# Performance work log

Measured on AMD Instinct MI355X. Metric: run time of the kernel, lower is better.

Reference implementation:

```python
import jax, jax.numpy as jnp
import numpy as np

WK = 5        # fine_window_size
STRIDE = 4    # hardcoded in forward
PAD = WK // 2


def _gather_windows(feat, b, idx):
    # feat: [N, C, H, W]; b, idx: [M]. Replicates F.unfold(k=5, s=4, p=2)
    # followed by permute/reshape(n, l, W^2, c) and advanced indexing,
    # but only materializes the M selected windows (fused unfold+gather).
    N, C, H, W = feat.shape
    out_w = (W + 2 * PAD - WK) // STRIDE + 1
    fp = jnp.pad(feat, ((0, 0), (0, 0), (PAD, PAD), (PAD, PAD)))
    gy = idx // out_w
    gx = idx % out_w
    rows = gy[:, None] * STRIDE + jnp.arange(WK)   # [M, WK]
    cols = gx[:, None] * STRIDE + jnp.arange(WK)   # [M, WK]
    # advanced indices at axes 0,2,3 with slice at axis 1 -> [M, WK, WK, C]
    patch = fp[b[:, None, None], :, rows[:, :, None], cols[:, None, :]]
    # F.unfold flattens channel-major (C, kh, kw); the torch code then
    # reshapes that C*WK*WK axis as (WK*WK, C) -- an index-mixing reshape
    # we must replicate exactly.
    M = b.shape[0]
    patch = patch.transpose(0, 3, 1, 2).reshape(M, C * WK * WK)
    return patch.reshape(M, WK * WK, C)


def setup_inputs() -> dict:
    key = jax.random.key(0)
    k0, k1, kb, ki, kj = jax.random.split(key, 5)
    N, C, H, W = 4, 128, 240, 320
    L = (H // STRIDE) * (W // STRIDE)  # 4800 coarse positions
    M = 6000
    return {
        "feat_f0": jax.random.normal(k0, (N, C, H, W), dtype=jnp.float32),
        "feat_f1": jax.random.normal(k1, (N, C, H, W), dtype=jnp.float32),
        "hw0_f": jnp.array([H, W], dtype=jnp.int64),
        "hw0_c": jnp.array([H // STRIDE, W // STRIDE], dtype=jnp.int64),
        "b_ids": jax.random.randint(kb, (M,), 0, N, dtype=jnp.int64),
        "i_ids": jax.random.randint(ki, (M,), 0, L, dtype=jnp.int64),
        "j_ids": jax.random.randint(kj, (M,), 0, L, dtype=jnp.int64),
    }


def reference(feat_f0, feat_f1, hw0_f, hw0_c, b_ids, i_ids, j_ids):
    feat0 = _gather_windows(feat_f0, b_ids, i_ids)  # [M, W^2, C]
    feat1 = _gather_windows(feat_f1, b_ids, j_ids)  # [M, W^2, C]
    return feat0, feat1
```

## Files before the change

### kernel.cpp

```cpp
#include <hip/hip_runtime.h>


#define MPTS 6000
#define NCH  128
#define FH   240
#define FW   320
#define OUTW 80
#define PTFLOATS (NCH * 25)

typedef float f2 __attribute__((ext_vector_type(2)));

__global__ __launch_bounds__(320) void fine_gather_kernel(
    const float* __restrict__ f0, const float* __restrict__ f1,
    const int* __restrict__ b_ids, const int* __restrict__ i_ids,
    const int* __restrict__ j_ids, float* __restrict__ out)
{
    __shared__ __align__(16) float lds[PTFLOATS];

    const int blk = blockIdx.x;
    const int map = blk >= MPTS;
    const int m   = map ? blk - MPTS : blk;
    const float* __restrict__ feat = map ? f1 : f0;
    const int idx = map ? j_ids[m] : i_ids[m];
    const int b   = b_ids[m];

    const int gy = idx / OUTW;
    const int gx = idx - gy * OUTW;
    const int row0 = gy * 4 - 2;
    const int col0 = gx * 4 - 2;

    const int t = threadIdx.x;

#pragma unroll
    for (int it = 0; it < 2; it++) {
        const int s = t + it * 320;
        const int c = s / 5;
        const int r = s - c * 5;
        const int row = row0 + r;
        const bool vrow = (row >= 0) & (row < FH);
        const float* src = feat + (((long)(b * NCH + c) * FH + row) * FW + col0);

        float v[5];
        if (vrow && (col0 >= 0)) {
            const f2* p = (const f2*)src;
            f2 a0 = p[0];
            f2 a1 = p[1];
            v[0] = a0.x; v[1] = a0.y; v[2] = a1.x; v[3] = a1.y;
            v[4] = src[4];
        } else {
#pragma unroll
            for (int k = 0; k < 5; k++) {
                const int cc = col0 + k;
                v[k] = (vrow && cc >= 0) ? src[k] : 0.0f;
            }
        }
        const int base = s * 5;
#pragma unroll
        for (int k = 0; k < 5; k++) lds[base + k] = v[k];
    }

    __syncthreads();

    float4* __restrict__ dst = (float4*)(out + (long)blk * PTFLOATS);
    const float4* sl = (const float4*)lds;
    for (int i = t; i < PTFLOATS / 4; i += 320)
        dst[i] = sl[i];
}

extern "C" void kernel_launch(void* const* d_in, const int* in_sizes, int n_in,
                              void* d_out, int out_size, void* d_ws, size_t ws_size,
                              hipStream_t stream) {
    const float* f0   = (const float*)d_in[0];
    const float* f1   = (const float*)d_in[1];
    const int* b_ids  = (const int*)d_in[4];
    const int* i_ids  = (const int*)d_in[5];
    const int* j_ids  = (const int*)d_in[6];
    float* out        = (float*)d_out;

    fine_gather_kernel<<<2 * MPTS, 320, 0, stream>>>(f0, f1, b_ids, i_ids, j_ids, out);
}
```

Baseline: 439.2 us.

## Sort gather blocks by image row band for cache locality, widen loads

Adds a counting sort (histogram, scan, scatter kernels) that orders the window-gather work by (map, batch, coarse row), so blocks touching nearby feature rows run together and share L2/MALL lines. Block IDs are remapped with an XCD-style interleave (blockIdx & 7) so that each of the eight chiplets receives a contiguous slice of the sorted order. The inner window load is changed from two float2 loads plus a scalar to two aligned float4 loads. The cost is four extra small kernel launches, and the change depends on workspace being available.

```diff
diff --git a/kernel.cpp b/kernel.cpp
--- a/kernel.cpp
+++ b/kernel.cpp
@@ -2,24 +2,94 @@
 
 
 #define MPTS 6000
+#define NPTS (2 * MPTS)
 #define NCH  128
 #define FH   240
 #define FW   320
 #define OUTW 80
+#define OUTH 60
+#define NKEY (2 * 4 * OUTH)
 #define PTFLOATS (NCH * 25)
 
+#define WS_HIST   0
+#define WS_CURSOR 512
+#define WS_BASE   1024
+#define WS_ORDER  2048
+#define WS_INTS   (WS_ORDER + NPTS)
+
 typedef float f2 __attribute__((ext_vector_type(2)));
+
+__device__ __forceinline__ int point_key(int map, int b, int gy) {
+    return (map * 4 + b) * OUTH + gy;
+}
+
+
+__global__ void k_zero(int* __restrict__ ws) {
+    const int t = threadIdx.x;
+    if (t < WS_BASE) ws[t] = 0;
+}
+
+__global__ void k_hist(const int* __restrict__ b_ids,
+                       const int* __restrict__ i_ids,
+                       const int* __restrict__ j_ids,
+                       int* __restrict__ ws) {
+    const int t = blockIdx.x * blockDim.x + threadIdx.x;
+    if (t >= NPTS) return;
+    const int map = t >= MPTS;
+    const int m   = map ? t - MPTS : t;
+    const int idx = map ? j_ids[m] : i_ids[m];
+    const int gy  = idx / OUTW;
+    atomicAdd(&ws[WS_HIST + point_key(map, b_ids[m], gy)], 1);
+}
+
+__global__ void k_scan(int* __restrict__ ws) {
+    __shared__ int h[NKEY];
+    const int t = threadIdx.x;
+    for (int i = t; i < NKEY; i += blockDim.x) h[i] = ws[WS_HIST + i];
+    __syncthreads();
+    if (t == 0) {
+        int acc = 0;
+        for (int i = 0; i < NKEY; i++) { int v = h[i]; h[i] = acc; acc += v; }
+    }
+    __syncthreads();
+    for (int i = t; i < NKEY; i += blockDim.x) ws[WS_BASE + i] = h[i];
+    if (t == 0) ws[WS_BASE + NKEY] = NPTS;
+}
+
+__global__ void k_scatter(const int* __restrict__ b_ids,
+                          const int* __restrict__ i_ids,
+                          const int* __restrict__ j_ids,
+                          int* __restrict__ ws) {
+    const int t = blockIdx.x * blockDim.x + threadIdx.x;
+    if (t >= NPTS) return;
+    const int map = t >= MPTS;
+    const int m   = map ? t - MPTS : t;
+    const int idx = map ? j_ids[m] : i_ids[m];
+    const int gy  = idx / OUTW;
+    const int key = point_key(map, b_ids[m], gy);
+    const int pos = atomicAdd(&ws[WS_CURSOR + key], 1);
+    ws[WS_ORDER + ws[WS_BASE + key] + pos] = t;
+}
+
 
 __global__ __launch_bounds__(320) void fine_gather_kernel(
     const float* __restrict__ f0, const float* __restrict__ f1,
     const int* __restrict__ b_ids, const int* __restrict__ i_ids,
-    const int* __restrict__ j_ids, float* __restrict__ out)
+    const int* __restrict__ j_ids, const int* __restrict__ order,
+    float* __restrict__ out)
 {
     __shared__ __align__(16) float lds[PTFLOATS];
 
-    const int blk = blockIdx.x;
-    const int map = blk >= MPTS;
-    const int m   = map ? blk - MPTS : blk;
+    int ent;
+    if (order) {
+        const int pos = (blockIdx.x & 7) * (NPTS / 8) + (blockIdx.x >> 3);
+        ent = order[pos];
+    } else {
+        ent = blockIdx.x;
+    }
+
+    const int map = ent >= MPTS;
+    const int m   = map ? ent - MPTS : ent;
     const float* __restrict__ feat = map ? f1 : f0;
     const int idx = map ? j_ids[m] : i_ids[m];
     const int b   = b_ids[m];
@@ -42,11 +112,10 @@
 
         float v[5];
         if (vrow && (col0 >= 0)) {
-            const f2* p = (const f2*)src;
-            f2 a0 = p[0];
-            f2 a1 = p[1];
-            v[0] = a0.x; v[1] = a0.y; v[2] = a1.x; v[3] = a1.y;
-            v[4] = src[4];
+            const float4* p = (const float4*)(src - 2);
+            const float4 q0 = p[0];
+            const float4 q1 = p[1];
+            v[0] = q0.z; v[1] = q0.w; v[2] = q1.x; v[3] = q1.y; v[4] = q1.z;
         } else {
 #pragma unroll
             for (int k = 0; k < 5; k++) {
@@ -61,11 +130,12 @@
 
     __syncthreads();
 
-    float4* __restrict__ dst = (float4*)(out + (long)blk * PTFLOATS);
+    float4* __restrict__ dst = (float4*)(out + (long)ent * PTFLOATS);
     const float4* sl = (const float4*)lds;
     for (int i = t; i < PTFLOATS / 4; i += 320)
         dst[i] = sl[i];
 }
+
 
 extern "C" void kernel_launch(void* const* d_in, const int* in_sizes, int n_in,
                               void* d_out, int out_size, void* d_ws, size_t ws_size,
@@ -77,5 +147,17 @@
     const int* j_ids  = (const int*)d_in[6];
     float* out        = (float*)d_out;
 
-    fine_gather_kernel<<<2 * MPTS, 320, 0, stream>>>(f0, f1, b_ids, i_ids, j_ids, out);
+    int* ws = (int*)d_ws;
+    const bool have_ws = (ws != nullptr) && (ws_size >= (size_t)WS_INTS * sizeof(int));
+
+    const int* order = nullptr;
+    if (have_ws) {
+        k_zero<<<1, 1024, 0, stream>>>(ws);
+        k_hist<<<(NPTS + 255) / 256, 256, 0, stream>>>(b_ids, i_ids, j_ids, ws);
+        k_scan<<<1, 512, 0, stream>>>(ws);
+        k_scatter<<<(NPTS + 255) / 256, 256, 0, stream>>>(b_ids, i_ids, j_ids, ws);
+        order = ws + WS_ORDER;
+    }
+
+    fine_gather_kernel<<<NPTS, 320, 0, stream>>>(f0, f1, b_ids, i_ids, j_ids, order, out);
 }
```

After: 405.6 us. -7.7%, faster.
